# Optimization experiments

Hardware: AMD Instinct MI355X
Metric: run time of the kernel (lower is better)

Reference implementation:

```python
import jax, jax.numpy as jnp
import numpy as np

NEG_SLOPE = 0.2  # PyG GATConv default negative_slope


def setup_inputs() -> dict:
    key = jax.random.key(0)
    ks = jax.random.split(key, 10)
    B, N, E = 8, 10000, 160000
    Din, Dout = 128, 128
    x = jax.random.normal(ks[0], (B, N, Din), dtype=jnp.float32)
    src = jax.random.randint(ks[1], (E,), 0, N)
    dst = jax.random.randint(ks[2], (E,), 0, N)
    edge_index = jnp.stack([src, dst])  # [2, E]
    edge_attr = jax.random.uniform(ks[3], (E,), dtype=jnp.float32)
    lim = 1.0 / np.sqrt(Din)
    W = jax.random.uniform(ks[4], (Dout, Din), jnp.float32, -lim, lim)   # shared lin (src==dst)
    We = jax.random.uniform(ks[5], (Dout, 1), jnp.float32, -1.0, 1.0)    # lin_edge, edge_dim=1
    att_src = jax.random.normal(ks[6], (Dout,), jnp.float32) * 0.1
    att_dst = jax.random.normal(ks[7], (Dout,), jnp.float32) * 0.1
    att_edge = jax.random.normal(ks[8], (Dout,), jnp.float32) * 0.1
    bias = jnp.zeros((Dout,), jnp.float32)
    return {"x": x, "edge_index": edge_index, "edge_attr": edge_attr,
            "W": W, "We": We, "att_src": att_src, "att_dst": att_dst,
            "att_edge": att_edge, "bias": bias}


def reference(x, edge_index, edge_attr, W, We, att_src, att_dst, att_edge, bias):
    B, N, Din = x.shape
    src, dst = edge_index[0], edge_index[1]
    # --- add self loops with fill_value='mean' (mean of incoming edge_attr per node) ---
    deg = jax.ops.segment_sum(jnp.ones_like(edge_attr), dst, num_segments=N)
    loop_attr = jax.ops.segment_sum(edge_attr, dst, num_segments=N) / jnp.maximum(deg, 1.0)
    ar = jnp.arange(N, dtype=src.dtype)
    full_src = jnp.concatenate([src, ar])          # [E2]
    full_dst = jnp.concatenate([dst, ar])          # [E2]
    full_attr = jnp.concatenate([edge_attr, loop_attr])
    # edge features: Linear(1 -> Dout, no bias) == outer product; identical across batch
    e_feat = full_attr[:, None] * We[:, 0][None, :]        # [E2, Dout]
    alpha_e = e_feat @ att_edge                            # [E2]

    def single(xb):  # xb: [N, Din]
        h = xb @ W.T                                       # [N, Dout]
        a_src = h @ att_src                                # [N]
        a_dst = h @ att_dst                                # [N]
        a = a_src[full_src] + a_dst[full_dst] + alpha_e    # [E2]
        a = jax.nn.leaky_relu(a, NEG_SLOPE)
        # segment softmax over destination node
        a_max = jax.ops.segment_max(a, full_dst, num_segments=N)
        a_max = jnp.where(jnp.isfinite(a_max), a_max, 0.0)
        ex = jnp.exp(a - a_max[full_dst])
        s = jax.ops.segment_sum(ex, full_dst, num_segments=N)
        alpha = ex / (s[full_dst] + 1e-16)                 # [E2]
        out = jax.ops.segment_sum(alpha[:, None] * h[full_src], full_dst, num_segments=N)
        return out + bias, alpha

    x_out, attn = jax.vmap(single)(x)   # [B, N, Dout], [B, E2]
    return x_out, attn
```

## Files before the change

kernel.cpp:

```cpp
#include <hip/hip_runtime.h>
#include <hip/hip_bf16.h>
#include <hip/hip_fp16.h>

typedef short short8 __attribute__((ext_vector_type(8)));
typedef float floatx4 __attribute__((ext_vector_type(4)));

static constexpr int BATCH = 8;
static constexpr int NN    = 10000;
static constexpr int EE    = 160000;
static constexpr int EE2   = EE + NN;
static constexpr int DD    = 128;
static constexpr int STR   = 64;
static constexpr float SLOPE = 0.2f;
static constexpr long OUT_ELEMS = (long)BATCH * NN * DD;
static constexpr int EB = EE / 256;

__device__ inline float ldf(const void* p, long i, int f32) {
    return f32 ? ((const float*)p)[i]
               : __bfloat162float(((const __hip_bfloat16*)p)[i]);
}
__device__ inline int esrc(const int* ei, int e, int i64) { return i64 ? ei[2 * e] : ei[e]; }
__device__ inline int edst(const int* ei, int e, int i64) { return i64 ? ei[2 * (EE + e)] : ei[EE + e]; }
__device__ inline short bf16bits(float v) {
    __hip_bfloat16 b = __float2bfloat16(v);
    short s; __builtin_memcpy(&s, &b, 2); return s;
}
__device__ inline short f16bits(float v) {
    __half b = __float2half(v);
    short s; __builtin_memcpy(&s, &b, 2); return s;
}

__global__ __launch_bounds__(256) void k_detect(const unsigned short* __restrict__ xu,
                                                const int* __restrict__ ei,
                                                const void* __restrict__ We,
                                                const void* __restrict__ att_edge,
                                                int* __restrict__ flags,
                                                float* __restrict__ cout,
                                                int* __restrict__ deg) {
    int t = threadIdx.x;
    if (blockIdx.x > 0) {
        int idx = (blockIdx.x - 1) * 256 + t;
        if (idx < NN) deg[idx] = 0;
        return;
    }
    __shared__ int cnt[2];
    __shared__ float red[256];
    if (t < 2) cnt[t] = 0;
    __syncthreads();
    int c1 = 0;
    for (int i = t; i < 32768; i += 256) {
        unsigned short u = xu[i];
        if ((u & 0x7F80u) == 0x7F80u) c1++;
    }
    int c2 = (ei[2 * t + 1] != 0) ? 1 : 0;
    if (c1) atomicAdd(&cnt[0], c1);
    if (c2) atomicAdd(&cnt[1], c2);
    __syncthreads();
    int f32 = (cnt[0] > 0);
    if (t == 0) { flags[0] = f32; flags[1] = (cnt[1] == 0); }
    red[t] = (t < DD) ? ldf(We, t, f32) * ldf(att_edge, t, f32) : 0.f;
    __syncthreads();
    for (int o = 128; o > 0; o >>= 1) {
        if (t < o) red[t] += red[t + o];
        __syncthreads();
    }
    if (t == 0) *cout = red[0];
}

__global__ __launch_bounds__(256) void k_bucket(const int* __restrict__ ei,
                                                const void* __restrict__ attr,
                                                const void* __restrict__ W,
                                                const int* __restrict__ flags,
                                                int* __restrict__ deg,
                                                int2* __restrict__ edgesP,
                                                __hip_bfloat16* __restrict__ Wb) {
    int f32 = flags[0], i64 = flags[1];
    int bId = blockIdx.x, t = threadIdx.x;
    if (bId < EB) {
        int e = bId * 256 + t;
        int d = edst(ei, e, i64);
        int s = esrc(ei, e, i64);
        float at = ldf(attr, e, f32);
        int p = atomicAdd(&deg[d], 1);
        if (p < STR) edgesP[d * STR + p] = make_int2(s, __float_as_int(at));
    } else {
        int idx = (bId - EB) * 512 + t * 2;
        if (f32) {
            float2 v = ((const float2*)W)[idx >> 1];
            Wb[idx]     = __float2bfloat16(v.x);
            Wb[idx + 1] = __float2bfloat16(v.y);
        } else {
            ((ushort2*)Wb)[idx >> 1] = ((const ushort2*)W)[idx >> 1];
        }
    }
}

template<int F32>
__device__ inline void load_a(const void* __restrict__ x, long row, int quad, short8 afr[4]) {
    if (F32) {
        const float* xr = (const float*)x + row * DD;
        #pragma unroll
        for (int kk = 0; kk < 4; kk++) {
            float4 f0 = *(const float4*)(xr + kk * 32 + quad * 8);
            float4 f1 = *(const float4*)(xr + kk * 32 + quad * 8 + 4);
            short8 a;
            a[0] = bf16bits(f0.x); a[1] = bf16bits(f0.y); a[2] = bf16bits(f0.z); a[3] = bf16bits(f0.w);
            a[4] = bf16bits(f1.x); a[5] = bf16bits(f1.y); a[6] = bf16bits(f1.z); a[7] = bf16bits(f1.w);
            afr[kk] = a;
        }
    } else {
        const short* xr = (const short*)x + row * DD;
        #pragma unroll
        for (int kk = 0; kk < 4; kk++)
            afr[kk] = *(const short8*)(xr + kk * 32 + quad * 8);
    }
}

__global__ __launch_bounds__(128) void k_gemm(const void* __restrict__ x,
                                              const __hip_bfloat16* __restrict__ Wb,
                                              const void* __restrict__ att_src,
                                              const void* __restrict__ att_dst,
                                              const int* __restrict__ flags,
                                              short* __restrict__ h,
                                              float* __restrict__ asrc_t, float* __restrict__ adst_t) {
    __shared__ float tile[2][16 * 132];
    int f32 = flags[0];
    int wave = threadIdx.x >> 6;
    int lane = threadIdx.x & 63;
    int l15  = lane & 15, quad = lane >> 4;
    long rows_base = (long)blockIdx.x * 32 + wave * 16;

    short8 afr[4];
    if (f32) load_a<1>(x, rows_base + l15, quad, afr);
    else     load_a<0>(x, rows_base + l15, quad, afr);

    const short* wr = (const short*)Wb;
    floatx4 acc[8];
    #pragma unroll
    for (int jt = 0; jt < 8; jt++) acc[jt] = (floatx4){0.f, 0.f, 0.f, 0.f};
    #pragma unroll
    for (int jt = 0; jt < 8; jt++) {
        #pragma unroll
        for (int kk = 0; kk < 4; kk++) {
            short8 bfr = *(const short8*)(wr + (jt * 16 + l15) * DD + kk * 32 + quad * 8);
            acc[jt] = __builtin_amdgcn_mfma_f32_16x16x32_bf16(afr[kk], bfr, acc[jt], 0, 0, 0);
        }
    }

    float asum[4] = {0.f, 0.f, 0.f, 0.f};
    float dsum[4] = {0.f, 0.f, 0.f, 0.f};
    #pragma unroll
    for (int jt = 0; jt < 8; jt++) {
        int col = jt * 16 + l15;
        float as = ldf(att_src, col, f32);
        float ad = ldf(att_dst, col, f32);
        #pragma unroll
        for (int r = 0; r < 4; r++) {
            asum[r] += acc[jt][r] * as;
            dsum[r] += acc[jt][r] * ad;
        }
    }
    #pragma unroll
    for (int r = 0; r < 4; r++) {
        float a = asum[r], d = dsum[r];
        #pragma unroll
        for (int o = 1; o < 16; o <<= 1) { a += __shfl_xor(a, o, 64); d += __shfl_xor(d, o, 64); }
        if (l15 == 0) {
            long row = rows_base + quad * 4 + r;
            int b = (int)(row / NN), n = (int)(row - (long)b * NN);
            asrc_t[n * 8 + b] = a;
            adst_t[n * 8 + b] = d;
        }
    }

    float* tl = &tile[wave][0];
    #pragma unroll
    for (int jt = 0; jt < 8; jt++)
        #pragma unroll
        for (int r = 0; r < 4; r++)
            tl[(quad * 4 + r) * 132 + jt * 16 + l15] = acc[jt][r];
    #pragma unroll
    for (int it = 0; it < 4; it++) {
        int row = it * 4 + quad;
        float4 f0 = *(const float4*)&tl[row * 132 + l15 * 8];
        float4 f1 = *(const float4*)&tl[row * 132 + l15 * 8 + 4];
        short8 o;
        o[0] = f16bits(f0.x); o[1] = f16bits(f0.y); o[2] = f16bits(f0.z); o[3] = f16bits(f0.w);
        o[4] = f16bits(f1.x); o[5] = f16bits(f1.y); o[6] = f16bits(f1.z); o[7] = f16bits(f1.w);
        *(short8*)(h + (rows_base + row) * DD + l15 * 8) = o;
    }
}

__global__ __launch_bounds__(256, 4) void k_agg(const int2* __restrict__ edgesP,
                                                const float* __restrict__ asrc_t,
                                                const float* __restrict__ adst_t,
                                                const __half* __restrict__ h,
                                                const int* __restrict__ deg,
                                                const float* __restrict__ cptr,
                                                const void* __restrict__ bias,
                                                const int* __restrict__ flags,
                                                float* __restrict__ invT,
                                                float* __restrict__ latc,
                                                void* __restrict__ outbuf) {
    __shared__ float4 smeta[16 * 36 + 16];
    int f32 = flags[0];
    int tid = threadIdx.x;
    int lane = tid & 63;
    int g   = lane >> 4;
    int c16 = tid & 15;
    int wv  = tid >> 6;
    int b = blockIdx.x & 7;
    int n = (blockIdx.x >> 3) * 16 + wv * 4 + g;

    float cc  = *cptr;
    int dg    = min(deg[n], STR);
    float an  = adst_t[n * 8 + b];

    const __half* hb = h + (long)b * NN * DD;
    float4* qptr = smeta + (wv * 4 + g) * 36;

    const int4* em4 = (const int4*)(edgesP + (long)n * STR);
    int4 mr0 = em4[c16];
    int4 mr1 = em4[16 + c16];

    float acc[8];
    #pragma unroll
    for (int j = 0; j < 8; j++) acc[j] = 0.f;
    float ssum = 0.f, sattr = 0.f;

#define STAGE(CH, MR)                                                        \
    {   int _e0 = (CH) * 32 + 2 * c16;                                       \
        bool _v0 = _e0 < dg, _v1 = (_e0 + 1) < dg;                           \
        int _s0 = _v0 ? MR.x : n;                                            \
        int _s1 = _v1 ? MR.z : n;                                            \
        float _at0 = _v0 ? __int_as_float(MR.y) : 0.f;                       \
        float _at1 = _v1 ? __int_as_float(MR.w) : 0.f;                       \
        float _ar0 = asrc_t[_s0 * 8 + b];                                    \
        float _ar1 = asrc_t[_s1 * 8 + b];                                    \
        float _a0 = fmaf(cc, _at0, _ar0 + an); _a0 = fmaxf(_a0, SLOPE * _a0);\
        float _a1 = fmaf(cc, _at1, _ar1 + an); _a1 = fmaxf(_a1, SLOPE * _a1);\
        float _ex0 = _v0 ? __expf(_a0) : 0.f;                                \
        float _ex1 = _v1 ? __expf(_a1) : 0.f;                                \
        ssum += _ex0 + _ex1; sattr += _at0 + _at1;                           \
        qptr[(CH) * 16 + c16] = make_float4(_ex0, __int_as_float(_s0),       \
                                            _ex1, __int_as_float(_s1));      \
    }

    STAGE(0, mr0);
    STAGE(1, mr1);

    int npq = (dg + 1) >> 1;
    int t1  = max(npq, __shfl_xor(npq, 16, 64));
    int npw = max(t1, __shfl_xor(t1, 32, 64));

#define DSR(S, MD)   MD = qptr[(S)];
#define HISS(MH, V0, V1)                                                     \
    {   int _s0 = __float_as_int(MH.y), _s1 = __float_as_int(MH.w);          \
        V0 = *(const uint4*)(hb + (long)_s0 * DD + c16 * 8);                 \
        V1 = *(const uint4*)(hb + (long)_s1 * DD + c16 * 8); }
#define FMA8(MF, V0, V1)                                                     \
    {   float _e0 = MF.x, _e1 = MF.z;                                        \
        const __half* _p0 = (const __half*)&V0;                              \
        const __half* _p1 = (const __half*)&V1;                              \
        _Pragma("unroll")                                                    \
        for (int _j = 0; _j < 8; _j++) acc[_j] += _e0 * __half2float(_p0[_j]);\
        _Pragma("unroll")                                                    \
        for (int _j = 0; _j < 8; _j++) acc[_j] += _e1 * __half2float(_p1[_j]);\
    }

    float4 m0, m1, m2, m3, m4, m5, m6, m7;
    uint4 hA0, hA1, hB0, hB1, hC0, hC1, hD0, hD1;
    DSR(0, m0); DSR(1, m1); DSR(2, m2); DSR(3, m3); DSR(4, m4); DSR(5, m5);
    HISS(m0, hA0, hA1); HISS(m1, hB0, hB1); HISS(m2, hC0, hC1);

    for (int p = 0; p < npw; p += 8) {
        DSR(p + 6,  m6); HISS(m3, hD0, hD1); FMA8(m0, hA0, hA1);
        if (p + 1 < npw) { DSR(p + 7,  m7); HISS(m4, hA0, hA1); FMA8(m1, hB0, hB1); }
        if (p + 2 < npw) { DSR(p + 8,  m0); HISS(m5, hB0, hB1); FMA8(m2, hC0, hC1); }
        if (p + 3 < npw) { DSR(p + 9,  m1); HISS(m6, hC0, hC1); FMA8(m3, hD0, hD1); }
        if (p + 4 < npw) { DSR(p + 10, m2); HISS(m7, hD0, hD1); FMA8(m4, hA0, hA1); }
        if (p + 5 < npw) { DSR(p + 11, m3); HISS(m0, hA0, hA1); FMA8(m5, hB0, hB1); }
        if (p + 6 < npw) { DSR(p + 12, m4); HISS(m1, hB0, hB1); FMA8(m6, hC0, hC1); }
        if (p + 7 < npw) { DSR(p + 13, m5); HISS(m2, hC0, hC1); FMA8(m7, hD0, hD1); }
    }
#undef STAGE
#undef DSR
#undef HISS
#undef FMA8

    #pragma unroll
    for (int o = 1; o < 16; o <<= 1) {
        ssum  += __shfl_xor(ssum, o, 64);
        sattr += __shfl_xor(sattr, o, 64);
    }

    float mean = sattr / fmaxf((float)dg, 1.0f);
    {
        float ars = asrc_t[n * 8 + b];
        float a = fmaf(cc, mean, ars + an);
        a = fmaxf(a, SLOPE * a);
        float ex = __expf(a);
        ssum += ex;
        uint4 hv = *(const uint4*)(hb + (long)n * DD + c16 * 8);
        const __half* hh = (const __half*)&hv;
        #pragma unroll
        for (int j = 0; j < 8; j++) acc[j] += ex * __half2float(hh[j]);
    }
    if (c16 == 0 && b == 0) latc[n] = mean;

    float inv = 1.0f / (ssum + 1e-16f);
    if (c16 == 0) invT[n * 8 + b] = inv;
    #pragma unroll
    for (int j = 0; j < 8; j++) acc[j] = acc[j] * inv + ldf(bias, c16 * 8 + j, f32);

    long row = (long)b * NN + n;
    if (f32) {
        float4 lo = {acc[0], acc[1], acc[2], acc[3]};
        float4 hi = {acc[4], acc[5], acc[6], acc[7]};
        float4* orow = (float4*)((float*)outbuf + row * DD);
        orow[c16 * 2]     = lo;
        orow[c16 * 2 + 1] = hi;
    } else {
        short8 o;
        #pragma unroll
        for (int j = 0; j < 8; j++) o[j] = bf16bits(acc[j]);
        ((short8*)((__hip_bfloat16*)outbuf + row * DD))[c16] = o;
    }
}

__global__ __launch_bounds__(256) void k_attn(const int* __restrict__ ei,
                                              const void* __restrict__ attr,
                                              const float* __restrict__ asrc_t,
                                              const float* __restrict__ adst_t,
                                              const float* __restrict__ latc,
                                              const float* __restrict__ cptr,
                                              const float* __restrict__ invT,
                                              const int* __restrict__ flags,
                                              void* __restrict__ outbuf) {
    int f32 = flags[0], i64 = flags[1];
    int e2 = blockIdx.x * 256 + threadIdx.x;
    if (e2 >= EE2) return;
    float c = *cptr;
    int s, d; float at;
    if (e2 < EE) {
        s = esrc(ei, e2, i64);
        d = edst(ei, e2, i64);
        at = ldf(attr, e2, f32);
    } else {
        int nn = e2 - EE;
        s = nn; d = nn;
        at = latc[nn];
    }
    float4 as0 = *(const float4*)(asrc_t + (long)s * 8);
    float4 as1 = *(const float4*)(asrc_t + (long)s * 8 + 4);
    float4 ad0 = *(const float4*)(adst_t + (long)d * 8);
    float4 ad1 = *(const float4*)(adst_t + (long)d * 8 + 4);
    float4 iv0 = *(const float4*)(invT   + (long)d * 8);
    float4 iv1 = *(const float4*)(invT   + (long)d * 8 + 4);
    float asv[8] = {as0.x, as0.y, as0.z, as0.w, as1.x, as1.y, as1.z, as1.w};
    float adv[8] = {ad0.x, ad0.y, ad0.z, ad0.w, ad1.x, ad1.y, ad1.z, ad1.w};
    float ivv[8] = {iv0.x, iv0.y, iv0.z, iv0.w, iv1.x, iv1.y, iv1.z, iv1.w};
    float ca = c * at;
    #pragma unroll
    for (int b = 0; b < BATCH; b++) {
        float a = asv[b] + adv[b] + ca;
        a = (a > 0.f) ? a : SLOPE * a;
        float al = __expf(a) * ivv[b];
        long gidx = OUT_ELEMS + (long)b * EE2 + e2;
        if (f32) ((float*)outbuf)[gidx] = al;
        else     ((__hip_bfloat16*)outbuf)[gidx] = __float2bfloat16(al);
    }
}

extern "C" void kernel_launch(void* const* d_in, const int* in_sizes, int n_in,
                              void* d_out, int out_size, void* d_ws, size_t ws_size,
                              hipStream_t stream) {
    const void* x        = d_in[0];
    const int*  ei       = (const int*)d_in[1];
    const void* attr     = d_in[2];
    const void* W        = d_in[3];
    const void* We       = d_in[4];
    const void* att_src  = d_in[5];
    const void* att_dst  = d_in[6];
    const void* att_edge = d_in[7];
    const void* bias     = d_in[8];

    char* ws = (char*)d_ws;
    size_t off = 0;
    auto alloc = [&](size_t bytes) { size_t o = off; off = (off + bytes + 255) & ~(size_t)255; return o; };
    short* h             = (short*)(ws + alloc((size_t)BATCH * NN * DD * 2));
    float* asrc_t        = (float*)(ws + alloc((size_t)NN * 8 * 4));
    float* adst_t        = (float*)(ws + alloc((size_t)NN * 8 * 4));
    float* invT          = (float*)(ws + alloc((size_t)NN * 8 * 4));
    int*   deg           = (int*)  (ws + alloc((size_t)NN * 4));
    float* latc          = (float*)(ws + alloc((size_t)NN * 4));
    int2*  edgesP        = (int2*) (ws + alloc((size_t)NN * STR * 8));
    __hip_bfloat16* Wb   = (__hip_bfloat16*)(ws + alloc((size_t)DD * DD * 2));
    float* cscal         = (float*)(ws + alloc(256));
    int*   flags         = (int*)  (ws + alloc(256));

    k_detect<<<41, 256, 0, stream>>>((const unsigned short*)x, ei, We, att_edge,
                                     flags, cscal, deg);
    k_bucket<<<EB + 32, 256, 0, stream>>>(ei, attr, W, flags, deg, edgesP, Wb);
    k_gemm  <<<(BATCH * NN) / 32, 128, 0, stream>>>(x, Wb, att_src, att_dst, flags,
                                                    h, asrc_t, adst_t);
    k_agg   <<<(BATCH * NN) / 16, 256, 0, stream>>>(edgesP, asrc_t, adst_t, (const __half*)h,
                                                    deg, cscal, bias, flags,
                                                    invT, latc, d_out);
    k_attn  <<<(EE2 + 255) / 256, 256, 0, stream>>>(ei, attr, asrc_t, adst_t, latc,
                                                    cscal, invT, flags, d_out);
}
```

Baseline: 223.2 us.

## Coalesce GEMM x loads via LDS, split attn by batch, trim agg loads

In k_gemm, fp32 x rows are now read coalesced across the wave, converted to bf16 and staged in shared memory before the MFMA fragments are loaded, replacing the strided per-lane fragment loads. k_attn gets a second grid dimension over batch, so each thread handles one batch entry instead of looping over eight. This adds parallelism, but the edge index and attribute loads are now repeated once per batch entry. k_agg skips the second edge-metadata load when a node has 32 or fewer incoming edges and uses 32-bit offset arithmetic for h gathers.

```diff
diff --git a/kernel.cpp b/kernel.cpp
--- a/kernel.cpp
+++ b/kernel.cpp
@@ -3,6 +3,7 @@
 #include <hip/hip_fp16.h>
 
 typedef short short8 __attribute__((ext_vector_type(8)));
+typedef short short4v __attribute__((ext_vector_type(4)));
 typedef float floatx4 __attribute__((ext_vector_type(4)));
 
 static constexpr int BATCH = 8;
@@ -95,27 +96,6 @@
     }
 }
 
-template<int F32>
-__device__ inline void load_a(const void* __restrict__ x, long row, int quad, short8 afr[4]) {
-    if (F32) {
-        const float* xr = (const float*)x + row * DD;
-        #pragma unroll
-        for (int kk = 0; kk < 4; kk++) {
-            float4 f0 = *(const float4*)(xr + kk * 32 + quad * 8);
-            float4 f1 = *(const float4*)(xr + kk * 32 + quad * 8 + 4);
-            short8 a;
-            a[0] = bf16bits(f0.x); a[1] = bf16bits(f0.y); a[2] = bf16bits(f0.z); a[3] = bf16bits(f0.w);
-            a[4] = bf16bits(f1.x); a[5] = bf16bits(f1.y); a[6] = bf16bits(f1.z); a[7] = bf16bits(f1.w);
-            afr[kk] = a;
-        }
-    } else {
-        const short* xr = (const short*)x + row * DD;
-        #pragma unroll
-        for (int kk = 0; kk < 4; kk++)
-            afr[kk] = *(const short8*)(xr + kk * 32 + quad * 8);
-    }
-}
-
 __global__ __launch_bounds__(128) void k_gemm(const void* __restrict__ x,
                                               const __hip_bfloat16* __restrict__ Wb,
                                               const void* __restrict__ att_src,
@@ -124,6 +104,7 @@
                                               short* __restrict__ h,
                                               float* __restrict__ asrc_t, float* __restrict__ adst_t) {
     __shared__ float tile[2][16 * 132];
+    __shared__ short tileS[2][16 * 132];
     int f32 = flags[0];
     int wave = threadIdx.x >> 6;
     int lane = threadIdx.x & 63;
@@ -131,8 +112,27 @@
     long rows_base = (long)blockIdx.x * 32 + wave * 16;
 
     short8 afr[4];
-    if (f32) load_a<1>(x, rows_base + l15, quad, afr);
-    else     load_a<0>(x, rows_base + l15, quad, afr);
+    if (f32) {
+        const float4* xs = (const float4*)((const float*)x + rows_base * DD);
+        short* st = &tileS[wave][0];
+        #pragma unroll
+        for (int j = 0; j < 8; j++) {
+            int v = lane + j * 64;
+            float4 f = xs[v];
+            short4v s4;
+            s4[0] = bf16bits(f.x); s4[1] = bf16bits(f.y);
+            s4[2] = bf16bits(f.z); s4[3] = bf16bits(f.w);
+            *(short4v*)&st[(v >> 5) * 132 + (v & 31) * 4] = s4;
+        }
+        #pragma unroll
+        for (int kk = 0; kk < 4; kk++)
+            afr[kk] = *(const short8*)&st[l15 * 132 + kk * 32 + quad * 8];
+    } else {
+        const short* xr = (const short*)x + (rows_base + l15) * DD;
+        #pragma unroll
+        for (int kk = 0; kk < 4; kk++)
+            afr[kk] = *(const short8*)(xr + kk * 32 + quad * 8);
+    }
 
     const short* wr = (const short*)Wb;
     floatx4 acc[8];
@@ -221,7 +221,9 @@
 
     const int4* em4 = (const int4*)(edgesP + (long)n * STR);
     int4 mr0 = em4[c16];
-    int4 mr1 = em4[16 + c16];
+    int4 mr1;
+    if (dg > 32) mr1 = em4[16 + c16];
+    else         mr1 = make_int4(n, 0, n, 0);
 
     float acc[8];
     #pragma unroll
@@ -255,9 +257,10 @@
 
 #define DSR(S, MD)   MD = qptr[(S)];
 #define HISS(MH, V0, V1)                                                     \
-    {   int _s0 = __float_as_int(MH.y), _s1 = __float_as_int(MH.w);          \
-        V0 = *(const uint4*)(hb + (long)_s0 * DD + c16 * 8);                 \
-        V1 = *(const uint4*)(hb + (long)_s1 * DD + c16 * 8); }
+    {   unsigned _o0 = (unsigned)__float_as_int(MH.y) * DD + c16 * 8;        \
+        unsigned _o1 = (unsigned)__float_as_int(MH.w) * DD + c16 * 8;        \
+        V0 = *(const uint4*)(hb + _o0);                                      \
+        V1 = *(const uint4*)(hb + _o1); }
 #define FMA8(MF, V0, V1)                                                     \
     {   float _e0 = MF.x, _e1 = MF.z;                                        \
         const __half* _p0 = (const __half*)&V0;                              \
@@ -301,7 +304,7 @@
         a = fmaxf(a, SLOPE * a);
         float ex = __expf(a);
         ssum += ex;
-        uint4 hv = *(const uint4*)(hb + (long)n * DD + c16 * 8);
+        uint4 hv = *(const uint4*)(hb + (unsigned)(n * DD + c16 * 8));
         const __half* hh = (const __half*)&hv;
         #pragma unroll
         for (int j = 0; j < 8; j++) acc[j] += ex * __half2float(hh[j]);
@@ -339,6 +342,7 @@
                                               void* __restrict__ outbuf) {
     int f32 = flags[0], i64 = flags[1];
     int e2 = blockIdx.x * 256 + threadIdx.x;
+    int b  = blockIdx.y;
     if (e2 >= EE2) return;
     float c = *cptr;
     int s, d; float at;
@@ -351,25 +355,12 @@
         s = nn; d = nn;
         at = latc[nn];
     }
-    float4 as0 = *(const float4*)(asrc_t + (long)s * 8);
-    float4 as1 = *(const float4*)(asrc_t + (long)s * 8 + 4);
-    float4 ad0 = *(const float4*)(adst_t + (long)d * 8);
-    float4 ad1 = *(const float4*)(adst_t + (long)d * 8 + 4);
-    float4 iv0 = *(const float4*)(invT   + (long)d * 8);
-    float4 iv1 = *(const float4*)(invT   + (long)d * 8 + 4);
-    float asv[8] = {as0.x, as0.y, as0.z, as0.w, as1.x, as1.y, as1.z, as1.w};
-    float adv[8] = {ad0.x, ad0.y, ad0.z, ad0.w, ad1.x, ad1.y, ad1.z, ad1.w};
-    float ivv[8] = {iv0.x, iv0.y, iv0.z, iv0.w, iv1.x, iv1.y, iv1.z, iv1.w};
-    float ca = c * at;
-    #pragma unroll
-    for (int b = 0; b < BATCH; b++) {
-        float a = asv[b] + adv[b] + ca;
-        a = (a > 0.f) ? a : SLOPE * a;
-        float al = __expf(a) * ivv[b];
-        long gidx = OUT_ELEMS + (long)b * EE2 + e2;
-        if (f32) ((float*)outbuf)[gidx] = al;
-        else     ((__hip_bfloat16*)outbuf)[gidx] = __float2bfloat16(al);
-    }
+    float a = asrc_t[s * 8 + b] + adst_t[d * 8 + b] + c * at;
+    a = (a > 0.f) ? a : SLOPE * a;
+    float al = __expf(a) * invT[d * 8 + b];
+    long gidx = OUT_ELEMS + (long)b * EE2 + e2;
+    if (f32) ((float*)outbuf)[gidx] = al;
+    else     ((__hip_bfloat16*)outbuf)[gidx] = __float2bfloat16(al);
 }
 
 extern "C" void kernel_launch(void* const* d_in, const int* in_sizes, int n_in,
@@ -407,6 +398,6 @@
     k_agg   <<<(BATCH * NN) / 16, 256, 0, stream>>>(edgesP, asrc_t, adst_t, (const __half*)h,
                                                     deg, cscal, bias, flags,
                                                     invT, latc, d_out);
-    k_attn  <<<(EE2 + 255) / 256, 256, 0, stream>>>(ei, attr, asrc_t, adst_t, latc,
-                                                    cscal, invT, flags, d_out);
-}
+    k_attn  <<<dim3((EE2 + 255) / 256, BATCH), 256, 0, stream>>>(ei, attr, asrc_t, adst_t, latc,
+                                                                 cscal, invT, flags, d_out);
+}
```

Measured after the change: 230.9 us. 3.5% more time.
